# Kernel optimization log

Hardware: AMD Instinct MI355X
Metric: run time of the kernel (lower is better)

The kernel has to match this reference:

```python
import jax, jax.numpy as jnp
import numpy as np

B, N_MAX, H, STEPS = 8, 36, 64, 5


def setup_inputs() -> dict:
    key = jax.random.key(0)
    ks = jax.random.split(key, 6)
    bound = 1.0 / np.sqrt(H)
    return {
        "edge_wgt": jax.random.normal(ks[0], (B, N_MAX, N_MAX, H, H), dtype=jnp.float32) * 0.1,
        "nodes_embed": jax.random.normal(ks[1], (B, N_MAX, H), dtype=jnp.float32),
        "mask": jnp.ones((B, N_MAX, 1), dtype=jnp.float32),
        "w_ih": jax.random.uniform(ks[2], (3 * H, H), jnp.float32, -bound, bound),
        "w_hh": jax.random.uniform(ks[3], (3 * H, H), jnp.float32, -bound, bound),
        "b_ih": jax.random.uniform(ks[4], (3 * H,), jnp.float32, -bound, bound),
        "b_hh": jax.random.uniform(ks[5], (3 * H,), jnp.float32, -bound, bound),
    }


def _gru_cell(x, h, w_ih, w_hh, b_ih, b_hh):
    # torch.nn.GRUCell math; x, h: [..., H]
    gi = x @ w_ih.T + b_ih
    gh = h @ w_hh.T + b_hh
    i_r, i_z, i_n = jnp.split(gi, 3, axis=-1)
    h_r, h_z, h_n = jnp.split(gh, 3, axis=-1)
    r = jax.nn.sigmoid(i_r + h_r)
    z = jax.nn.sigmoid(i_z + h_z)
    n = jnp.tanh(i_n + r * h_n)
    return (1.0 - z) * n + z * h


def reference(edge_wgt, nodes_embed, mask, w_ih, w_hh, b_ih, b_hh):
    n_max = edge_wgt.shape[1]
    inv_n2 = 1.0 / (n_max * n_max)
    nodes = nodes_embed
    for _ in range(STEPS):
        # messages[b,j,k] = (1/n^2) * sum_{i,l} edge_wgt[b,i,j,k,l] * nodes[b,i,l]
        messages = jnp.einsum('bijkl,bil->bjk', edge_wgt, nodes) * inv_n2
        nodes = _gru_cell(messages, nodes, w_ih, w_hh, b_ih, b_hh) * mask
    return nodes
```

## Files before the change

### kernel.cpp

```cpp
#include <hip/hip_runtime.h>
#include <hip/hip_bf16.h>


#define BB 8
#define NN 36
#define HH 64
#define WAVES 4
#define IPW (NN / WAVES)
#define NBJ (BB * NN)
#define INVN2 (1.0f / (float)(NN * NN))

__device__ __forceinline__ unsigned bf16rtn(float f) {
    unsigned u = __float_as_uint(f);
    return (u + 0x7FFFu + ((u >> 16) & 1u)) >> 16;
}

__device__ __forceinline__ float gru_lane(
    const float* __restrict__ ms, const float* __restrict__ hs, int t,
    const float* __restrict__ w_ih, const float* __restrict__ w_hh,
    const float* __restrict__ b_ih, const float* __restrict__ b_hh)
{
    float gi0 = b_ih[t], gi1 = b_ih[HH + t], gi2 = b_ih[2 * HH + t];
    float gh0 = b_hh[t], gh1 = b_hh[HH + t], gh2 = b_hh[2 * HH + t];

    const float4* __restrict__ wi0 = (const float4*)(w_ih + (0 * HH + t) * HH);
    const float4* __restrict__ wi1 = (const float4*)(w_ih + (1 * HH + t) * HH);
    const float4* __restrict__ wi2 = (const float4*)(w_ih + (2 * HH + t) * HH);
    const float4* __restrict__ wh0 = (const float4*)(w_hh + (0 * HH + t) * HH);
    const float4* __restrict__ wh1 = (const float4*)(w_hh + (1 * HH + t) * HH);
    const float4* __restrict__ wh2 = (const float4*)(w_hh + (2 * HH + t) * HH);

    #pragma unroll
    for (int k4 = 0; k4 < HH / 4; ++k4) {
        const float4 mv = *(const float4*)&ms[k4 * 4];
        const float4 hv = *(const float4*)&hs[k4 * 4];
        float4 a;
        a = wi0[k4]; gi0 += a.x * mv.x + a.y * mv.y + a.z * mv.z + a.w * mv.w;
        a = wi1[k4]; gi1 += a.x * mv.x + a.y * mv.y + a.z * mv.z + a.w * mv.w;
        a = wi2[k4]; gi2 += a.x * mv.x + a.y * mv.y + a.z * mv.z + a.w * mv.w;
        a = wh0[k4]; gh0 += a.x * hv.x + a.y * hv.y + a.z * hv.z + a.w * hv.w;
        a = wh1[k4]; gh1 += a.x * hv.x + a.y * hv.y + a.z * hv.z + a.w * hv.w;
        a = wh2[k4]; gh2 += a.x * hv.x + a.y * hv.y + a.z * hv.z + a.w * hv.w;
    }
    const float r = 1.f / (1.f + expf(-(gi0 + gh0)));
    const float z = 1.f / (1.f + expf(-(gi1 + gh1)));
    const float n = tanhf(gi2 + r * gh2);
    return (1.f - z) * n + z * hs[t];
}

__global__ __launch_bounds__(256, 2) void step1_f32(
    const float* __restrict__ edge,
    const float* __restrict__ nodes_in,
    uint2* __restrict__ ebf,
    const float* __restrict__ mask,
    const float* __restrict__ w_ih, const float* __restrict__ w_hh,
    const float* __restrict__ b_ih, const float* __restrict__ b_hh,
    float* __restrict__ nodes_out)
{
    const int tid  = threadIdx.x;
    const int lane = tid & 63;
    const int wv   = tid >> 6;
    const int bj = blockIdx.x;
    const int j  = bj % NN;
    const int b  = bj / NN;

    __shared__ float part[WAVES][HH];
    __shared__ float ms[HH];
    __shared__ float hs[HH];

    const int l4 = lane & 15;

    float acc[16];
    #pragma unroll
    for (int it = 0; it < 16; ++it) acc[it] = 0.f;

    for (int ii = 0; ii < IPW; ++ii) {
        const int i = wv * IPW + ii;
        const float4 v = *(const float4*)(nodes_in + (b * NN + i) * HH + l4 * 4);
        const size_t blkElem = (size_t)((b * NN + i) * NN + j) * (HH * HH);
        const float4* __restrict__ Wb = (const float4*)(edge + blkElem);
        uint2* __restrict__ Eb = ebf + (blkElem >> 2);
        #pragma unroll
        for (int it = 0; it < 16; ++it) {
            const float4 w = Wb[it * 64 + lane];
            acc[it] = fmaf(w.x, v.x, acc[it]);
            acc[it] = fmaf(w.y, v.y, acc[it]);
            acc[it] = fmaf(w.z, v.z, acc[it]);
            acc[it] = fmaf(w.w, v.w, acc[it]);
            uint2 pk;
            pk.x = bf16rtn(w.x) | (bf16rtn(w.y) << 16);
            pk.y = bf16rtn(w.z) | (bf16rtn(w.w) << 16);
            Eb[it * 64 + lane] = pk;
        }
    }

    #pragma unroll
    for (int m = 1; m < 16; m <<= 1) {
        #pragma unroll
        for (int it = 0; it < 16; ++it)
            acc[it] += __shfl_xor(acc[it], m, 64);
    }

    const int p  = lane & 15;
    const int gq = lane >> 4;
    float outv = acc[0];
    #pragma unroll
    for (int t = 1; t < 16; ++t) outv = (p == t) ? acc[t] : outv;
    part[wv][4 * p + gq] = outv;

    __syncthreads();

    if (tid < HH) {
        const float m = part[0][tid] + part[1][tid] + part[2][tid] + part[3][tid];
        ms[tid] = m * INVN2;
        hs[tid] = nodes_in[bj * HH + tid];
    }
    __syncthreads();

    if (tid < HH) {
        const float o = gru_lane(ms, hs, tid, w_ih, w_hh, b_ih, b_hh);
        nodes_out[bj * HH + tid] = o * mask[bj];
    }
}

__global__ __launch_bounds__(256, 2) void step_bf16(
    const uint4* __restrict__ ebf,
    const float* __restrict__ nodes_in,
    const float* __restrict__ mask,
    const float* __restrict__ w_ih, const float* __restrict__ w_hh,
    const float* __restrict__ b_ih, const float* __restrict__ b_hh,
    float* __restrict__ nodes_out)
{
    const int tid  = threadIdx.x;
    const int lane = tid & 63;
    const int wv   = tid >> 6;
    const int bj = blockIdx.x;
    const int j  = bj % NN;
    const int b  = bj / NN;

    __shared__ float part[WAVES][HH];
    __shared__ float ms[HH];
    __shared__ float hs[HH];

    const int l8 = lane & 7;

    float acc[8];
    #pragma unroll
    for (int it = 0; it < 8; ++it) acc[it] = 0.f;

    for (int ii = 0; ii < IPW; ++ii) {
        const int i = wv * IPW + ii;
        const float* np_ = nodes_in + (b * NN + i) * HH + l8 * 8;
        const float4 v0 = *(const float4*)(np_);
        const float4 v1 = *(const float4*)(np_ + 4);
        const size_t blkElem = (size_t)((b * NN + i) * NN + j) * (HH * HH);
        const uint4* __restrict__ Wb = ebf + (blkElem >> 3);
        #pragma unroll
        for (int it = 0; it < 8; ++it) {
            const uint4 w = Wb[it * 64 + lane];
            acc[it] = fmaf(__uint_as_float(w.x << 16),          v0.x, acc[it]);
            acc[it] = fmaf(__uint_as_float(w.x & 0xffff0000u),  v0.y, acc[it]);
            acc[it] = fmaf(__uint_as_float(w.y << 16),          v0.z, acc[it]);
            acc[it] = fmaf(__uint_as_float(w.y & 0xffff0000u),  v0.w, acc[it]);
            acc[it] = fmaf(__uint_as_float(w.z << 16),          v1.x, acc[it]);
            acc[it] = fmaf(__uint_as_float(w.z & 0xffff0000u),  v1.y, acc[it]);
            acc[it] = fmaf(__uint_as_float(w.w << 16),          v1.z, acc[it]);
            acc[it] = fmaf(__uint_as_float(w.w & 0xffff0000u),  v1.w, acc[it]);
        }
    }

    #pragma unroll
    for (int m = 1; m < 8; m <<= 1) {
        #pragma unroll
        for (int it = 0; it < 8; ++it)
            acc[it] += __shfl_xor(acc[it], m, 64);
    }

    const int p  = lane & 7;
    const int gq = lane >> 3;
    float outv = acc[0];
    #pragma unroll
    for (int tt = 1; tt < 8; ++tt) outv = (p == tt) ? acc[tt] : outv;
    part[wv][8 * p + gq] = outv;

    __syncthreads();

    if (tid < HH) {
        const float m = part[0][tid] + part[1][tid] + part[2][tid] + part[3][tid];
        ms[tid] = m * INVN2;
        hs[tid] = nodes_in[bj * HH + tid];
    }
    __syncthreads();

    if (tid < HH) {
        const float o = gru_lane(ms, hs, tid, w_ih, w_hh, b_ih, b_hh);
        nodes_out[bj * HH + tid] = o * mask[bj];
    }
}

extern "C" void kernel_launch(void* const* d_in, const int* in_sizes, int n_in,
                              void* d_out, int out_size, void* d_ws, size_t ws_size,
                              hipStream_t stream) {
    const float* edge   = (const float*)d_in[0];
    const float* nodes0 = (const float*)d_in[1];
    const float* mask   = (const float*)d_in[2];
    const float* w_ih   = (const float*)d_in[3];
    const float* w_hh   = (const float*)d_in[4];
    const float* b_ih   = (const float*)d_in[5];
    const float* b_hh   = (const float*)d_in[6];
    float* out = (float*)d_out;

    float* ws = (float*)d_ws;
    const int nodes_elems = BB * NN * HH;
    float* nodesA = ws;
    float* nodesB = ws + nodes_elems;
    float* ebf_f  = ws + 2 * nodes_elems;
    uint2* ebf2 = (uint2*)ebf_f;
    const uint4* ebf4 = (const uint4*)ebf_f;

    step1_f32<<<NBJ, 256, 0, stream>>>(edge, nodes0, ebf2, mask,
                                       w_ih, w_hh, b_ih, b_hh, nodesA);
    step_bf16<<<NBJ, 256, 0, stream>>>(ebf4, nodesA, mask,
                                       w_ih, w_hh, b_ih, b_hh, nodesB);
    step_bf16<<<NBJ, 256, 0, stream>>>(ebf4, nodesB, mask,
                                       w_ih, w_hh, b_ih, b_hh, nodesA);
    step_bf16<<<NBJ, 256, 0, stream>>>(ebf4, nodesA, mask,
                                       w_ih, w_hh, b_ih, b_hh, nodesB);
    step_bf16<<<NBJ, 256, 0, stream>>>(ebf4, nodesB, mask,
                                       w_ih, w_hh, b_ih, b_hh, out);
}
```

Baseline: 143.0 us.

## Split first-step einsum across more blocks with separate GRU reduction kernel

After: 144.5 us. No clear change (+1.0%).

```diff
diff --git a/kernel.cpp b/kernel.cpp
--- a/kernel.cpp
+++ b/kernel.cpp
@@ -5,6 +5,8 @@
 #define BB 8
 #define NN 36
 #define HH 64
+#define GG 12
+#define IPG (NN / GG)
 #define WAVES 4
 #define IPW (NN / WAVES)
 #define NBJ (BB * NN)
@@ -48,25 +50,17 @@
     return (1.f - z) * n + z * hs[t];
 }
 
-__global__ __launch_bounds__(256, 2) void step1_f32(
+__global__ __launch_bounds__(64) void einsum_f32_cvt(
     const float* __restrict__ edge,
-    const float* __restrict__ nodes_in,
-    uint2* __restrict__ ebf,
-    const float* __restrict__ mask,
-    const float* __restrict__ w_ih, const float* __restrict__ w_hh,
-    const float* __restrict__ b_ih, const float* __restrict__ b_hh,
-    float* __restrict__ nodes_out)
-{
-    const int tid  = threadIdx.x;
-    const int lane = tid & 63;
-    const int wv   = tid >> 6;
-    const int bj = blockIdx.x;
-    const int j  = bj % NN;
-    const int b  = bj / NN;
-
-    __shared__ float part[WAVES][HH];
-    __shared__ float ms[HH];
-    __shared__ float hs[HH];
+    const float* __restrict__ nodes,
+    float* __restrict__ partial,
+    uint2* __restrict__ ebf)
+{
+    const int lane = threadIdx.x;
+    const int bid  = blockIdx.x;
+    const int g = bid % GG;
+    const int j = (bid / GG) % NN;
+    const int b = bid / (GG * NN);
 
     const int l4 = lane & 15;
 
@@ -74,9 +68,10 @@
     #pragma unroll
     for (int it = 0; it < 16; ++it) acc[it] = 0.f;
 
-    for (int ii = 0; ii < IPW; ++ii) {
-        const int i = wv * IPW + ii;
-        const float4 v = *(const float4*)(nodes_in + (b * NN + i) * HH + l4 * 4);
+    #pragma unroll
+    for (int ii = 0; ii < IPG; ++ii) {
+        const int i = g * IPG + ii;
+        const float4 v = *(const float4*)(nodes + (b * NN + i) * HH + l4 * 4);
         const size_t blkElem = (size_t)((b * NN + i) * NN + j) * (HH * HH);
         const float4* __restrict__ Wb = (const float4*)(edge + blkElem);
         uint2* __restrict__ Eb = ebf + (blkElem >> 2);
@@ -106,21 +101,34 @@
     float outv = acc[0];
     #pragma unroll
     for (int t = 1; t < 16; ++t) outv = (p == t) ? acc[t] : outv;
-    part[wv][4 * p + gq] = outv;
-
+
+    partial[(size_t)bid * HH + (4 * p + gq)] = outv;
+}
+
+__global__ __launch_bounds__(64) void gru_step(
+    const float* __restrict__ partial,
+    const float* __restrict__ nodes_in,
+    const float* __restrict__ mask,
+    const float* __restrict__ w_ih, const float* __restrict__ w_hh,
+    const float* __restrict__ b_ih, const float* __restrict__ b_hh,
+    float* __restrict__ nodes_out)
+{
+    const int t  = threadIdx.x;
+    const int bj = blockIdx.x;
+
+    float m = 0.f;
+    #pragma unroll
+    for (int g = 0; g < GG; ++g)
+        m += partial[((size_t)bj * GG + g) * HH + t];
+
+    __shared__ float ms[HH];
+    __shared__ float hs[HH];
+    ms[t] = m * INVN2;
+    hs[t] = nodes_in[bj * HH + t];
     __syncthreads();
 
-    if (tid < HH) {
-        const float m = part[0][tid] + part[1][tid] + part[2][tid] + part[3][tid];
-        ms[tid] = m * INVN2;
-        hs[tid] = nodes_in[bj * HH + tid];
-    }
-    __syncthreads();
-
-    if (tid < HH) {
-        const float o = gru_lane(ms, hs, tid, w_ih, w_hh, b_ih, b_hh);
-        nodes_out[bj * HH + tid] = o * mask[bj];
-    }
+    const float o = gru_lane(ms, hs, t, w_ih, w_hh, b_ih, b_hh);
+    nodes_out[bj * HH + t] = o * mask[bj];
 }
 
 __global__ __launch_bounds__(256, 2) void step_bf16(
@@ -211,15 +219,18 @@
     float* out = (float*)d_out;
 
     float* ws = (float*)d_ws;
-    const int nodes_elems = BB * NN * HH;
-    float* nodesA = ws;
-    float* nodesB = ws + nodes_elems;
-    float* ebf_f  = ws + 2 * nodes_elems;
+    const int nodes_elems   = BB * NN * HH;
+    const int partial_elems = NBJ * GG * HH;
+    float* nodesA  = ws;
+    float* nodesB  = ws + nodes_elems;
+    float* partial = ws + 2 * nodes_elems;
+    float* ebf_f   = partial + partial_elems;
     uint2* ebf2 = (uint2*)ebf_f;
     const uint4* ebf4 = (const uint4*)ebf_f;
 
-    step1_f32<<<NBJ, 256, 0, stream>>>(edge, nodes0, ebf2, mask,
-                                       w_ih, w_hh, b_ih, b_hh, nodesA);
+    einsum_f32_cvt<<<NBJ * GG, 64, 0, stream>>>(edge, nodes0, partial, ebf2);
+    gru_step<<<NBJ, 64, 0, stream>>>(partial, nodes0, mask,
+                                     w_ih, w_hh, b_ih, b_hh, nodesA);
     step_bf16<<<NBJ, 256, 0, stream>>>(ebf4, nodesA, mask,
                                        w_ih, w_hh, b_ih, b_hh, nodesB);
     step_bf16<<<NBJ, 256, 0, stream>>>(ebf4, nodesB, mask,
```
